# Kernel tuning notes

Hardware: AMD Instinct MI355X
Metric: run time of the kernel (lower is better)

## Reference

```python
import jax, jax.numpy as jnp
import numpy as np

S, B, E = 1024, 64, 1024   # src_seq_len, batch, encoder_hidden_size
H, A = 1024, 1024          # decoder hidden, attention dim
EMB, V = 512, 32000        # embedding_dim, output vocab


def setup_inputs() -> dict:
    key = jax.random.key(0)
    ks = jax.random.split(key, 16)
    sd = lambda n: 1.0 / np.sqrt(n)
    u = lambda k, shape, n: jax.random.uniform(k, shape, jnp.float32, -sd(n), sd(n))
    return {
        "prev_y": jax.random.normal(ks[0], (B, EMB), jnp.float32),
        "prev_h": jax.random.normal(ks[1], (1, B, H), jnp.float32),
        "enc_out": jax.random.normal(ks[2], (S, B, E), jnp.float32),
        # attention params
        "U_w": u(ks[3], (A, E), E), "U_b": u(ks[4], (A,), E),
        "W_w": u(ks[5], (A, H), H), "W_b": u(ks[6], (A,), H),
        "v_w": u(ks[7], (1, A), A), "v_b": u(ks[8], (1,), A),
        # combine + GRU + output params
        "Wc_w": u(ks[9], (H, EMB + E), EMB + E), "Wc_b": u(ks[10], (H,), EMB + E),
        "W_ih": u(ks[11], (3 * H, H), H), "W_hh": u(ks[12], (3 * H, H), H),
        "b_ih": u(ks[13], (3 * H,), H), "b_hh": u(ks[14], (3 * H,), H),
        "Wout_w": u(ks[15], (V, H), H), "Wout_b": jnp.zeros((V,), jnp.float32),
        "mask": 768,
    }


def reference(prev_y, prev_h, enc_out, U_w, U_b, W_w, W_b, v_w, v_b,
              Wc_w, Wc_b, W_ih, W_hh, b_ih, b_hh, Wout_w, Wout_b, mask):
    s, b, e = enc_out.shape
    h = prev_h[0]                                     # [B,H]
    # --- additive (Bahdanau) attention with multiplicative 0/1 prefix mask ---
    uh = jnp.einsum('sbe,ae->sba', enc_out, U_w) + U_b  # [S,B,A]
    wq = h @ W_w.T + W_b                                # [B,A]
    scores = (jnp.tanh(uh + wq) @ v_w[0] + v_b[0]).T    # [B,S]
    m = min(int(mask), s)
    mask_vec = (jnp.arange(s) < m).astype(scores.dtype) # [S]
    scores = scores * mask_vec                          # multiply, NOT -inf (faithful)
    attn = jax.nn.softmax(scores, axis=1)               # [B,S]
    ctx = jnp.einsum('bs,sbe->be', attn, enc_out)       # [B,E]
    # --- combine + single GRU step (PyTorch gate order r,z,n) ---
    x = jnp.concatenate([prev_y, ctx], axis=1) @ Wc_w.T + Wc_b  # [B,H]
    gi = x @ W_ih.T + b_ih                              # [B,3H]
    gh = h @ W_hh.T + b_hh
    Hh = h.shape[1]
    r = jax.nn.sigmoid(gi[:, :Hh] + gh[:, :Hh])
    z = jax.nn.sigmoid(gi[:, Hh:2 * Hh] + gh[:, Hh:2 * Hh])
    n = jnp.tanh(gi[:, 2 * Hh:] + r * gh[:, 2 * Hh:])
    h_new = (1.0 - z) * n + z * h                       # [B,H]
    # --- output projection + log-softmax ---
    logits = h_new @ Wout_w.T + Wout_b                  # [B,V]
    dec_output = jax.nn.log_softmax(logits, axis=1)
    return dec_output, h_new[None], attn
```

## Files before the change

kernel.cpp:

```cpp
#include <hip/hip_runtime.h>

typedef float f32x4 __attribute__((ext_vector_type(4)));
typedef short short8 __attribute__((ext_vector_type(8)));

#define SEQ   1024
#define BB    64
#define VOCAB 32000

__device__ __forceinline__ unsigned short f2bf(float f){
  union { float f; unsigned u; } v; v.f = f;
  unsigned r = v.u + 0x7FFFu + ((v.u >> 16) & 1u);
  return (unsigned short)(r >> 16);
}
__device__ __forceinline__ unsigned pk2(float a, float b){
  return (unsigned)f2bf(a) | ((unsigned)f2bf(b) << 16);
}
__device__ __forceinline__ float tanh_fast(float x){
  float a = fminf(fmaxf(x, -15.f), 15.f);
  float e = __expf(2.f * a);
  return (e - 1.f) / (e + 1.f);
}
__device__ __forceinline__ float sigm(float x){ return 1.f / (1.f + expf(-x)); }

__device__ __forceinline__ void ld4(float4* dst, const float* p){
  const float4* q = (const float4*)p;
  dst[0]=q[0]; dst[1]=q[1]; dst[2]=q[2]; dst[3]=q[3];
}
__device__ __forceinline__ void cvt_store(char* base, int row, int kb0, const float4* f){
  int xs = (row & 7) << 4;
  uint4 u;
  u.x = pk2(f[0].x, f[0].y); u.y = pk2(f[0].z, f[0].w);
  u.z = pk2(f[1].x, f[1].y); u.w = pk2(f[1].z, f[1].w);
  *(uint4*)(base + row*128 + (kb0 ^ xs)) = u;
  u.x = pk2(f[2].x, f[2].y); u.y = pk2(f[2].z, f[2].w);
  u.z = pk2(f[3].x, f[3].y); u.w = pk2(f[3].z, f[3].w);
  *(uint4*)(base + row*128 + ((kb0 + 16) ^ xs)) = u;
}

__global__ __launch_bounds__(256, 2)
void score_gemm(const float* __restrict__ enc, const float* __restrict__ Uw,
                const float* __restrict__ Ub, const float* __restrict__ vw,
                const float* __restrict__ wqm, const int* __restrict__ maskp,
                float* __restrict__ scores)
{
  __shared__ char smem[65536];
  int m = *maskp; m = m < 0 ? 0 : (m > SEQ ? SEQ : m);
  int cx = blockIdx.x & 7, jj = blockIdx.x >> 3;
  int mtile = (jj & ~7) | cx;
  int ntile = jj & 7;
  if (mtile * 2 >= m) return;
  int row0 = mtile * 128;
  int t = threadIdx.x, lane = t & 63;
  int wid = t >> 6, wm = wid >> 1, wn = wid & 1;
  int srow = t >> 2;
  int sk4 = (t & 3) << 4;
  int kb0 = (t & 3) << 5;

  const float* Ag0 = enc + (size_t)(row0 + srow) * 1024 + sk4;
  const float* Ag1 = Ag0 + 64 * 1024;
  const float* Bg0 = Uw  + (size_t)(ntile * 128 + srow) * 1024 + sk4;
  const float* Bg1 = Bg0 + 64 * 1024;

  float4 fa0[4], fa1[4], fb0[4], fb1[4];

  int aAddr[4], bAddr[4], aXor[4], bXor[4];
  #pragma unroll
  for (int i = 0; i < 4; ++i){
    int ra = wm*64 + i*16 + (lane & 15);
    aAddr[i] = ra * 128; aXor[i] = (ra & 7) << 4;
    int rb = wn*64 + i*16 + (lane & 15);
    bAddr[i] = rb * 128; bXor[i] = (rb & 7) << 4;
  }
  int klane = (lane >> 4) << 4;

  f32x4 acc[4][4] = {};

  ld4(fa0, Ag0); ld4(fa1, Ag1); ld4(fb0, Bg0); ld4(fb1, Bg1);
  {
    char* bA = smem; char* bB = smem + 16384;
    cvt_store(bA, srow,      kb0, fa0);
    cvt_store(bA, srow + 64, kb0, fa1);
    cvt_store(bB, srow,      kb0, fb0);
    cvt_store(bB, srow + 64, kb0, fb1);
  }

  #pragma unroll 2
  for (int ks = 0; ks < 16; ++ks){
    int buf = ks & 1;
    if (ks < 15){
      int ko = (ks + 1) * 64;
      ld4(fa0, Ag0 + ko); ld4(fa1, Ag1 + ko);
      ld4(fb0, Bg0 + ko); ld4(fb1, Bg1 + ko);
    }
    __syncthreads();
    {
      char* bA = smem + buf * 32768;
      char* bB = bA + 16384;
      #pragma unroll
      for (int kk = 0; kk < 2; ++kk){
        short8 af[4], bv[4];
        int kb = kk * 64 + klane;
        #pragma unroll
        for (int i = 0; i < 4; ++i){
          af[i] = *(const short8*)(bA + aAddr[i] + (kb ^ aXor[i]));
          bv[i] = *(const short8*)(bB + bAddr[i] + (kb ^ bXor[i]));
        }
        #pragma unroll
        for (int mi = 0; mi < 4; ++mi)
          #pragma unroll
          for (int ni = 0; ni < 4; ++ni)
            acc[mi][ni] = __builtin_amdgcn_mfma_f32_16x16x32_bf16(af[mi], bv[ni], acc[mi][ni], 0, 0, 0);
      }
    }
    if (ks < 15){
      int nb = buf ^ 1;
      char* bA = smem + nb * 32768; char* bB = bA + 16384;
      cvt_store(bA, srow,      kb0, fa0);
      cvt_store(bA, srow + 64, kb0, fa1);
      cvt_store(bB, srow,      kb0, fb0);
      cvt_store(bB, srow + 64, kb0, fb1);
    }
  }

  int s_idx = mtile * 2 + wm;
  if (s_idx < m){
    float ubv[4], vwv[4];
    #pragma unroll
    for (int ni = 0; ni < 4; ++ni){
      int nt = ntile*128 + wn*64 + ni*16 + (lane & 15);
      ubv[ni] = Ub[nt]; vwv[ni] = vw[nt];
    }
    #pragma unroll
    for (int mi = 0; mi < 4; ++mi){
      #pragma unroll
      for (int j = 0; j < 4; ++j){
        int b = mi*16 + ((lane >> 4) << 2) + j;
        const float* wqrow = wqm + b * 1024;
        float asum = 0.f;
        #pragma unroll
        for (int ni = 0; ni < 4; ++ni){
          int nt = ntile*128 + wn*64 + ni*16 + (lane & 15);
          float uh = acc[mi][ni][j] + ubv[ni] + wqrow[nt];
          asum += tanh_fast(uh) * vwv[ni];
        }
        asum += __shfl_xor(asum, 1, 64);
        asum += __shfl_xor(asum, 2, 64);
        asum += __shfl_xor(asum, 4, 64);
        asum += __shfl_xor(asum, 8, 64);
        if ((lane & 15) == 0)
          atomicAdd(scores + b * 1024 + s_idx, asum);
      }
    }
  }
}

__global__ __launch_bounds__(256)
void gemm_m64(const float* __restrict__ A, const float* __restrict__ Bw,
              const float* __restrict__ bias, float* __restrict__ C,
              int N, int K, int stepsPerZ)
{
  __shared__ unsigned short sA[2][64 * 40];
  __shared__ unsigned short sB[2][128 * 40];
  int t = threadIdx.x, lane = t & 63, wid = t >> 6;
  int ntile = blockIdx.x, z = blockIdx.z;
  int arow = t >> 2, ak = (t & 3) * 8;
  int brow = t >> 1, bk = (t & 1) * 16;
  const float* Ap = A + (size_t)arow * K + ak + (size_t)z * stepsPerZ * 32;
  const float* Bp = Bw + (size_t)(ntile * 128 + brow) * K + bk + (size_t)z * stepsPerZ * 32;
  int klane = (lane >> 4) << 4;
  f32x4 acc[4][2] = {};
  float4 a0, a1, b0, b1, b2, b3;

  {
    const float4* pa = (const float4*)Ap;
    a0 = pa[0]; a1 = pa[1];
    const float4* pb = (const float4*)Bp;
    b0 = pb[0]; b1 = pb[1]; b2 = pb[2]; b3 = pb[3];
    uint4 u;
    u.x = pk2(a0.x,a0.y); u.y = pk2(a0.z,a0.w);
    u.z = pk2(a1.x,a1.y); u.w = pk2(a1.z,a1.w);
    *(uint4*)((char*)sA[0] + arow*80 + ak*2) = u;
    u.x = pk2(b0.x,b0.y); u.y = pk2(b0.z,b0.w);
    u.z = pk2(b1.x,b1.y); u.w = pk2(b1.z,b1.w);
    *(uint4*)((char*)sB[0] + brow*80 + bk*2) = u;
    u.x = pk2(b2.x,b2.y); u.y = pk2(b2.z,b2.w);
    u.z = pk2(b3.x,b3.y); u.w = pk2(b3.z,b3.w);
    *(uint4*)((char*)sB[0] + brow*80 + bk*2 + 16) = u;
  }

  for (int ks = 0; ks < stepsPerZ; ++ks){
    int buf = ks & 1;
    if (ks + 1 < stepsPerZ){
      int kg = (ks + 1) * 32;
      const float4* pa = (const float4*)(Ap + kg);
      a0 = pa[0]; a1 = pa[1];
      const float4* pb = (const float4*)(Bp + kg);
      b0 = pb[0]; b1 = pb[1]; b2 = pb[2]; b3 = pb[3];
    }
    __syncthreads();
    {
      short8 af[4], bv[2];
      #pragma unroll
      for (int mi = 0; mi < 4; ++mi)
        af[mi] = *(const short8*)((char*)sA[buf] + (mi*16 + (lane & 15))*80 + klane);
      #pragma unroll
      for (int ni = 0; ni < 2; ++ni)
        bv[ni] = *(const short8*)((char*)sB[buf] + (wid*32 + ni*16 + (lane & 15))*80 + klane);
      #pragma unroll
      for (int mi = 0; mi < 4; ++mi)
        #pragma unroll
        for (int ni = 0; ni < 2; ++ni)
          acc[mi][ni] = __builtin_amdgcn_mfma_f32_16x16x32_bf16(af[mi], bv[ni], acc[mi][ni], 0, 0, 0);
    }
    if (ks + 1 < stepsPerZ){
      int nb = buf ^ 1;
      uint4 u;
      u.x = pk2(a0.x,a0.y); u.y = pk2(a0.z,a0.w);
      u.z = pk2(a1.x,a1.y); u.w = pk2(a1.z,a1.w);
      *(uint4*)((char*)sA[nb] + arow*80 + ak*2) = u;
      u.x = pk2(b0.x,b0.y); u.y = pk2(b0.z,b0.w);
      u.z = pk2(b1.x,b1.y); u.w = pk2(b1.z,b1.w);
      *(uint4*)((char*)sB[nb] + brow*80 + bk*2) = u;
      u.x = pk2(b2.x,b2.y); u.y = pk2(b2.z,b2.w);
      u.z = pk2(b3.x,b3.y); u.w = pk2(b3.z,b3.w);
      *(uint4*)((char*)sB[nb] + brow*80 + bk*2 + 16) = u;
    }
  }

  bool multi = (gridDim.z > 1);
  #pragma unroll
  for (int ni = 0; ni < 2; ++ni){
    int cg = ntile*128 + wid*32 + ni*16 + (lane & 15);
    float bz = 0.f;
    if (bias && (!multi || z == 0)) bz = bias[cg];
    #pragma unroll
    for (int mi = 0; mi < 4; ++mi){
      int r0 = mi*16 + ((lane >> 4) << 2);
      #pragma unroll
      for (int j = 0; j < 4; ++j){
        float val = acc[mi][ni][j] + bz;
        int off = (r0 + j) * N + cg;
        if (multi) atomicAdd(C + off, val);
        else       C[off] = val;
      }
    }
  }
}

__global__ __launch_bounds__(256)
void softmax_attn(const float* __restrict__ scores, const float* __restrict__ vb,
                  const int* __restrict__ maskp, float* __restrict__ attn)
{
  __shared__ float sb[4];
  int b = blockIdx.x, t = threadIdx.x, lane = t & 63, wid = t >> 6;
  int m = *maskp; m = m < 0 ? 0 : (m > SEQ ? SEQ : m);
  float vb0 = vb[0];
  float v[4]; float mx = -1e30f;
  #pragma unroll
  for (int k = 0; k < 4; ++k){
    int s = t + k * 256;
    float x = (s < m) ? scores[b*1024 + s] + vb0 : 0.f;
    v[k] = x; mx = fmaxf(mx, x);
  }
  for (int d = 1; d < 64; d <<= 1) mx = fmaxf(mx, __shfl_xor(mx, d, 64));
  if (lane == 0) sb[wid] = mx;
  __syncthreads();
  mx = fmaxf(fmaxf(sb[0], sb[1]), fmaxf(sb[2], sb[3]));
  float sum = 0.f;
  #pragma unroll
  for (int k = 0; k < 4; ++k){ v[k] = expf(v[k] - mx); sum += v[k]; }
  for (int d = 1; d < 64; d <<= 1) sum += __shfl_xor(sum, d, 64);
  __syncthreads();
  if (lane == 0) sb[wid] = sum;
  __syncthreads();
  sum = sb[0] + sb[1] + sb[2] + sb[3];
  #pragma unroll
  for (int k = 0; k < 4; ++k) attn[b*1024 + t + k*256] = v[k] / sum;
}

__global__ __launch_bounds__(256)
void ctx_atomic(const float* __restrict__ attn, const float* __restrict__ enc,
                float* __restrict__ xcat)
{
  int b = blockIdx.x >> 4, ch = blockIdx.x & 15;
  int t = threadIdx.x;
  __shared__ float a_s[64];
  if (t < 64) a_s[t] = attn[b*1024 + ch*64 + t];
  __syncthreads();
  const float* ep = enc + (size_t)(ch * 64) * 65536 + b * 1024 + t * 4;
  f32x4 acc = {};
  for (int s2 = 0; s2 < 64; ++s2){
    f32x4 v = *(const f32x4*)(ep + (size_t)s2 * 65536);
    acc += a_s[s2] * v;
  }
  float* dst = xcat + (size_t)b * 1536 + 512 + t * 4;
  atomicAdd(dst + 0, acc.x);
  atomicAdd(dst + 1, acc.y);
  atomicAdd(dst + 2, acc.z);
  atomicAdd(dst + 3, acc.w);
}

__global__ __launch_bounds__(128)
void copy_py(const float* __restrict__ py, float* __restrict__ xcat)
{
  int b = blockIdx.x, t = threadIdx.x;
  *(f32x4*)(xcat + (size_t)b*1536 + t*4) = *(const f32x4*)(py + (size_t)b*512 + t*4);
}

__global__ __launch_bounds__(256)
void gru_kernel(const float* __restrict__ gi, const float* __restrict__ gh,
                const float* __restrict__ h, float* __restrict__ hnew)
{
  int idx = blockIdx.x * 256 + threadIdx.x;
  int b = idx >> 10, i = idx & 1023;
  const float* gib = gi + b*3072; const float* ghb = gh + b*3072;
  float r = sigm(gib[i] + ghb[i]);
  float z = sigm(gib[1024 + i] + ghb[1024 + i]);
  float n = tanhf(gib[2048 + i] + r * ghb[2048 + i]);
  hnew[idx] = (1.f - z) * n + z * h[idx];
}

__global__ __launch_bounds__(1024)
void logsoftmax_kernel(float* __restrict__ logits)
{
  __shared__ float sb[16];
  int b = blockIdx.x, t = threadIdx.x, lane = t & 63, wid = t >> 6;
  float* row = logits + (size_t)b * VOCAB;
  float v[32]; float mx = -1e30f;
  #pragma unroll
  for (int k = 0; k < 32; ++k){
    int idx = t + k * 1024;
    if (idx < VOCAB){ v[k] = row[idx]; mx = fmaxf(mx, v[k]); }
    else v[k] = -1e30f;
  }
  for (int d = 1; d < 64; d <<= 1) mx = fmaxf(mx, __shfl_xor(mx, d, 64));
  if (lane == 0) sb[wid] = mx;
  __syncthreads();
  float m2 = -1e30f;
  for (int i = 0; i < 16; ++i) m2 = fmaxf(m2, sb[i]);
  mx = m2;
  float sum = 0.f;
  #pragma unroll
  for (int k = 0; k < 32; ++k){
    int idx = t + k * 1024;
    if (idx < VOCAB) sum += expf(v[k] - mx);
  }
  for (int d = 1; d < 64; d <<= 1) sum += __shfl_xor(sum, d, 64);
  __syncthreads();
  if (lane == 0) sb[wid] = sum;
  __syncthreads();
  float s2 = 0.f;
  for (int i = 0; i < 16; ++i) s2 += sb[i];
  float lse = mx + logf(s2);
  #pragma unroll
  for (int k = 0; k < 32; ++k){
    int idx = t + k * 1024;
    if (idx < VOCAB) row[idx] = v[k] - lse;
  }
}

extern "C" void kernel_launch(void* const* d_in, const int* in_sizes, int n_in,
                              void* d_out, int out_size, void* d_ws, size_t ws_size,
                              hipStream_t stream)
{
  const float* prev_y = (const float*)d_in[0];
  const float* prev_h = (const float*)d_in[1];
  const float* enc    = (const float*)d_in[2];
  const float* U_w    = (const float*)d_in[3];
  const float* U_b    = (const float*)d_in[4];
  const float* W_w    = (const float*)d_in[5];
  const float* W_b    = (const float*)d_in[6];
  const float* v_w    = (const float*)d_in[7];
  const float* v_b    = (const float*)d_in[8];
  const float* Wc_w   = (const float*)d_in[9];
  const float* Wc_b   = (const float*)d_in[10];
  const float* W_ih   = (const float*)d_in[11];
  const float* W_hh   = (const float*)d_in[12];
  const float* b_ih   = (const float*)d_in[13];
  const float* b_hh   = (const float*)d_in[14];
  const float* Wout_w = (const float*)d_in[15];
  const float* Wout_b = (const float*)d_in[16];
  const int*   maskp  = (const int*)d_in[17];

  float* ws     = (float*)d_ws;
  float* scores = ws;
  float* wq     = ws + 65536;
  float* xcat   = ws + 131072;
  float* xvec   = ws + 229376;
  float* gi     = ws + 294912;
  float* gh     = ws + 491520;

  float* out_logp = (float*)d_out;
  float* out_h    = out_logp + 64 * VOCAB;
  float* out_attn = out_h + 65536;

  hipMemsetAsync(d_ws, 0, (size_t)688128 * sizeof(float), stream);

  gemm_m64<<<dim3(8, 1, 8), 256, 0, stream>>>(prev_h, W_w, W_b, wq, 1024, 1024, 4);
  score_gemm<<<4096, 256, 0, stream>>>(enc, U_w, U_b, v_w, wq, maskp, scores);
  softmax_attn<<<64, 256, 0, stream>>>(scores, v_b, maskp, out_attn);
  ctx_atomic<<<1024, 256, 0, stream>>>(out_attn, enc, xcat);
  copy_py<<<64, 128, 0, stream>>>(prev_y, xcat);
  gemm_m64<<<dim3(8, 1, 8), 256, 0, stream>>>(xcat, Wc_w, Wc_b, xvec, 1024, 1536, 6);
  gemm_m64<<<dim3(24, 1, 8), 256, 0, stream>>>(xvec, W_ih, b_ih, gi, 3072, 1024, 4);
  gemm_m64<<<dim3(24, 1, 8), 256, 0, stream>>>(prev_h, W_hh, b_hh, gh, 3072, 1024, 4);
  gru_kernel<<<256, 256, 0, stream>>>(gi, gh, prev_h, out_h);
  gemm_m64<<<dim3(250, 1, 1), 256, 0, stream>>>(out_h, Wout_w, Wout_b, out_logp, VOCAB, 1024, 32);
  logsoftmax_kernel<<<64, 1024, 0, stream>>>(out_logp);
}
```

Measured before the change: 827.0 us.

## Pre-convert enc/U_w to bf16, use direct LDS loads, replace atomics with partial buffers

```diff
diff --git a/kernel.cpp b/kernel.cpp
--- a/kernel.cpp
+++ b/kernel.cpp
@@ -2,9 +2,9 @@
 
 typedef float f32x4 __attribute__((ext_vector_type(4)));
 typedef short short8 __attribute__((ext_vector_type(8)));
+typedef unsigned int u32;
 
 #define SEQ   1024
-#define BB    64
 #define VOCAB 32000
 
 __device__ __forceinline__ unsigned short f2bf(float f){
@@ -14,6 +14,9 @@
 }
 __device__ __forceinline__ unsigned pk2(float a, float b){
   return (unsigned)f2bf(a) | ((unsigned)f2bf(b) << 16);
+}
+__device__ __forceinline__ float bf2f(unsigned short h){
+  union { unsigned u; float f; } v; v.u = ((unsigned)h) << 16; return v.f;
 }
 __device__ __forceinline__ float tanh_fast(float x){
   float a = fminf(fmaxf(x, -15.f), 15.f);
@@ -36,32 +39,48 @@
   u.z = pk2(f[3].x, f[3].y); u.w = pk2(f[3].z, f[3].w);
   *(uint4*)(base + row*128 + ((kb0 + 16) ^ xs)) = u;
 }
-
-__global__ __launch_bounds__(256, 2)
-void score_gemm(const float* __restrict__ enc, const float* __restrict__ Uw,
-                const float* __restrict__ Ub, const float* __restrict__ vw,
-                const float* __restrict__ wqm, const int* __restrict__ maskp,
-                float* __restrict__ scores)
-{
-  __shared__ char smem[65536];
+__device__ __forceinline__ void gload_lds16(const void* g, void* l){
+  __builtin_amdgcn_global_load_lds((const __attribute__((address_space(1))) u32*)g,
+                                   (__attribute__((address_space(3))) u32*)l, 16, 0, 0);
+}
+
+__global__ __launch_bounds__(256)
+void convert_all(const float* __restrict__ uw, const float* __restrict__ enc,
+                 unsigned short* __restrict__ uwb, unsigned short* __restrict__ encb)
+{
+  const int UWC = 131072;
+  const int TOT = UWC + 8388608;
+  int stride = gridDim.x * 256;
+  for (int c = blockIdx.x*256 + threadIdx.x; c < TOT; c += stride){
+    const float* src; unsigned short* dst;
+    if (c < UWC){ src = uw + (size_t)c*8;        dst = uwb + (size_t)c*8; }
+    else        { size_t e = (size_t)(c-UWC)*8;  src = enc + e; dst = encb + e; }
+    float4 f0 = ((const float4*)src)[0], f1 = ((const float4*)src)[1];
+    uint4 u;
+    u.x = pk2(f0.x,f0.y); u.y = pk2(f0.z,f0.w);
+    u.z = pk2(f1.x,f1.y); u.w = pk2(f1.z,f1.w);
+    *(uint4*)dst = u;
+  }
+}
+
+__global__ __launch_bounds__(256)
+void score_gemm_bf16(const unsigned short* __restrict__ encb,
+                     const unsigned short* __restrict__ uwb,
+                     const float* __restrict__ Ub, const float* __restrict__ vw,
+                     const float* __restrict__ wqm, const int* __restrict__ maskp,
+                     float* __restrict__ scores_part)
+{
+  __shared__ char smem[32768];
   int m = *maskp; m = m < 0 ? 0 : (m > SEQ ? SEQ : m);
-  int cx = blockIdx.x & 7, jj = blockIdx.x >> 3;
-  int mtile = (jj & ~7) | cx;
-  int ntile = jj & 7;
+  int bI = blockIdx.x;
+  int mtile = bI & 511, ntile = bI >> 9;
   if (mtile * 2 >= m) return;
-  int row0 = mtile * 128;
-  int t = threadIdx.x, lane = t & 63;
-  int wid = t >> 6, wm = wid >> 1, wn = wid & 1;
-  int srow = t >> 2;
-  int sk4 = (t & 3) << 4;
-  int kb0 = (t & 3) << 5;
-
-  const float* Ag0 = enc + (size_t)(row0 + srow) * 1024 + sk4;
-  const float* Ag1 = Ag0 + 64 * 1024;
-  const float* Bg0 = Uw  + (size_t)(ntile * 128 + srow) * 1024 + sk4;
-  const float* Bg1 = Bg0 + 64 * 1024;
-
-  float4 fa0[4], fa1[4], fb0[4], fb1[4];
+  int t = threadIdx.x, lane = t & 63, wid = t >> 6;
+  int wm = wid >> 1, wn = wid & 1;
+
+  int cswz = (((lane & 7) ^ (lane >> 3)) << 4);
+  const char* pa = (const char*)encb + ((size_t)(mtile*128 + wid*8 + (lane>>3)))*2048 + cswz;
+  const char* pb = (const char*)uwb  + ((size_t)(ntile*128 + wid*8 + (lane>>3)))*2048 + cswz;
 
   int aAddr[4], bAddr[4], aXor[4], bXor[4];
   #pragma unroll
@@ -74,51 +93,30 @@
   int klane = (lane >> 4) << 4;
 
   f32x4 acc[4][4] = {};
-
-  ld4(fa0, Ag0); ld4(fa1, Ag1); ld4(fb0, Bg0); ld4(fb1, Bg1);
-  {
-    char* bA = smem; char* bB = smem + 16384;
-    cvt_store(bA, srow,      kb0, fa0);
-    cvt_store(bA, srow + 64, kb0, fa1);
-    cvt_store(bB, srow,      kb0, fb0);
-    cvt_store(bB, srow + 64, kb0, fb1);
-  }
-
-  #pragma unroll 2
+  char* bA = smem; char* bB = smem + 16384;
+
   for (int ks = 0; ks < 16; ++ks){
-    int buf = ks & 1;
-    if (ks < 15){
-      int ko = (ks + 1) * 64;
-      ld4(fa0, Ag0 + ko); ld4(fa1, Ag1 + ko);
-      ld4(fb0, Bg0 + ko); ld4(fb1, Bg1 + ko);
-    }
     __syncthreads();
-    {
-      char* bA = smem + buf * 32768;
-      char* bB = bA + 16384;
-      #pragma unroll
-      for (int kk = 0; kk < 2; ++kk){
-        short8 af[4], bv[4];
-        int kb = kk * 64 + klane;
+    #pragma unroll
+    for (int i = 0; i < 4; ++i){
+      gload_lds16(pa + (size_t)i*65536 + ks*128, bA + (i*4 + wid)*1024);
+      gload_lds16(pb + (size_t)i*65536 + ks*128, bB + (i*4 + wid)*1024);
+    }
+    __syncthreads();
+    #pragma unroll
+    for (int kk = 0; kk < 2; ++kk){
+      short8 af[4], bv[4];
+      int kb = kk * 64 + klane;
+      #pragma unroll
+      for (int i = 0; i < 4; ++i){
+        af[i] = *(const short8*)(bA + aAddr[i] + (kb ^ aXor[i]));
+        bv[i] = *(const short8*)(bB + bAddr[i] + (kb ^ bXor[i]));
+      }
+      #pragma unroll
+      for (int mi = 0; mi < 4; ++mi)
         #pragma unroll
-        for (int i = 0; i < 4; ++i){
-          af[i] = *(const short8*)(bA + aAddr[i] + (kb ^ aXor[i]));
-          bv[i] = *(const short8*)(bB + bAddr[i] + (kb ^ bXor[i]));
-        }
-        #pragma unroll
-        for (int mi = 0; mi < 4; ++mi)
-          #pragma unroll
-          for (int ni = 0; ni < 4; ++ni)
-            acc[mi][ni] = __builtin_amdgcn_mfma_f32_16x16x32_bf16(af[mi], bv[ni], acc[mi][ni], 0, 0, 0);
-      }
-    }
-    if (ks < 15){
-      int nb = buf ^ 1;
-      char* bA = smem + nb * 32768; char* bB = bA + 16384;
-      cvt_store(bA, srow,      kb0, fa0);
-      cvt_store(bA, srow + 64, kb0, fa1);
-      cvt_store(bB, srow,      kb0, fb0);
-      cvt_store(bB, srow + 64, kb0, fb1);
+        for (int ni = 0; ni < 4; ++ni)
+          acc[mi][ni] = __builtin_amdgcn_mfma_f32_16x16x32_bf16(af[mi], bv[ni], acc[mi][ni], 0, 0, 0);
     }
   }
 
@@ -148,7 +146,120 @@
         asum += __shfl_xor(asum, 4, 64);
         asum += __shfl_xor(asum, 8, 64);
         if ((lane & 15) == 0)
-          atomicAdd(scores + b * 1024 + s_idx, asum);
+          scores_part[(ntile*2 + wn)*65536 + s_idx*64 + b] = asum;
+      }
+    }
+  }
+}
+
+__global__ __launch_bounds__(256, 2)
+void score_gemm_f32(const float* __restrict__ enc, const float* __restrict__ Uw,
+                    const float* __restrict__ Ub, const float* __restrict__ vw,
+                    const float* __restrict__ wqm, const int* __restrict__ maskp,
+                    float* __restrict__ scores_part)
+{
+  __shared__ char smem[65536];
+  int m = *maskp; m = m < 0 ? 0 : (m > SEQ ? SEQ : m);
+  int bI = blockIdx.x;
+  int mtile = bI & 511, ntile = bI >> 9;
+  if (mtile * 2 >= m) return;
+  int row0 = mtile * 128;
+  int t = threadIdx.x, lane = t & 63;
+  int wid = t >> 6, wm = wid >> 1, wn = wid & 1;
+  int srow = t >> 2;
+  int sk4 = (t & 3) << 4;
+  int kb0 = (t & 3) << 5;
+
+  const float* Ag0 = enc + (size_t)(row0 + srow) * 1024 + sk4;
+  const float* Ag1 = Ag0 + 64 * 1024;
+  const float* Bg0 = Uw  + (size_t)(ntile * 128 + srow) * 1024 + sk4;
+  const float* Bg1 = Bg0 + 64 * 1024;
+
+  float4 fa0[4], fa1[4], fb0[4], fb1[4];
+  int aAddr[4], bAddr[4], aXor[4], bXor[4];
+  #pragma unroll
+  for (int i = 0; i < 4; ++i){
+    int ra = wm*64 + i*16 + (lane & 15);
+    aAddr[i] = ra * 128; aXor[i] = (ra & 7) << 4;
+    int rb = wn*64 + i*16 + (lane & 15);
+    bAddr[i] = rb * 128; bXor[i] = (rb & 7) << 4;
+  }
+  int klane = (lane >> 4) << 4;
+  f32x4 acc[4][4] = {};
+
+  ld4(fa0, Ag0); ld4(fa1, Ag1); ld4(fb0, Bg0); ld4(fb1, Bg1);
+  {
+    char* bA = smem; char* bB = smem + 16384;
+    cvt_store(bA, srow,      kb0, fa0);
+    cvt_store(bA, srow + 64, kb0, fa1);
+    cvt_store(bB, srow,      kb0, fb0);
+    cvt_store(bB, srow + 64, kb0, fb1);
+  }
+  #pragma unroll 2
+  for (int ks = 0; ks < 16; ++ks){
+    int buf = ks & 1;
+    if (ks < 15){
+      int ko = (ks + 1) * 64;
+      ld4(fa0, Ag0 + ko); ld4(fa1, Ag1 + ko);
+      ld4(fb0, Bg0 + ko); ld4(fb1, Bg1 + ko);
+    }
+    __syncthreads();
+    {
+      char* bA = smem + buf * 32768;
+      char* bB = bA + 16384;
+      #pragma unroll
+      for (int kk = 0; kk < 2; ++kk){
+        short8 af[4], bv[4];
+        int kb = kk * 64 + klane;
+        #pragma unroll
+        for (int i = 0; i < 4; ++i){
+          af[i] = *(const short8*)(bA + aAddr[i] + (kb ^ aXor[i]));
+          bv[i] = *(const short8*)(bB + bAddr[i] + (kb ^ bXor[i]));
+        }
+        #pragma unroll
+        for (int mi = 0; mi < 4; ++mi)
+          #pragma unroll
+          for (int ni = 0; ni < 4; ++ni)
+            acc[mi][ni] = __builtin_amdgcn_mfma_f32_16x16x32_bf16(af[mi], bv[ni], acc[mi][ni], 0, 0, 0);
+      }
+    }
+    if (ks < 15){
+      int nb = buf ^ 1;
+      char* bA = smem + nb * 32768; char* bB = bA + 16384;
+      cvt_store(bA, srow,      kb0, fa0);
+      cvt_store(bA, srow + 64, kb0, fa1);
+      cvt_store(bB, srow,      kb0, fb0);
+      cvt_store(bB, srow + 64, kb0, fb1);
+    }
+  }
+
+  int s_idx = mtile * 2 + wm;
+  if (s_idx < m){
+    float ubv[4], vwv[4];
+    #pragma unroll
+    for (int ni = 0; ni < 4; ++ni){
+      int nt = ntile*128 + wn*64 + ni*16 + (lane & 15);
+      ubv[ni] = Ub[nt]; vwv[ni] = vw[nt];
+    }
+    #pragma unroll
+    for (int mi = 0; mi < 4; ++mi){
+      #pragma unroll
+      for (int j = 0; j < 4; ++j){
+        int b = mi*16 + ((lane >> 4) << 2) + j;
+        const float* wqrow = wqm + b * 1024;
+        float asum = 0.f;
+        #pragma unroll
+        for (int ni = 0; ni < 4; ++ni){
+          int nt = ntile*128 + wn*64 + ni*16 + (lane & 15);
+          float uh = acc[mi][ni][j] + ubv[ni] + wqrow[nt];
+          asum += tanh_fast(uh) * vwv[ni];
+        }
+        asum += __shfl_xor(asum, 1, 64);
+        asum += __shfl_xor(asum, 2, 64);
+        asum += __shfl_xor(asum, 4, 64);
+        asum += __shfl_xor(asum, 8, 64);
+        if ((lane & 15) == 0)
+          scores_part[(ntile*2 + wn)*65536 + s_idx*64 + b] = asum;
       }
     }
   }
@@ -157,7 +268,7 @@
 __global__ __launch_bounds__(256)
 void gemm_m64(const float* __restrict__ A, const float* __restrict__ Bw,
               const float* __restrict__ bias, float* __restrict__ C,
-              int N, int K, int stepsPerZ)
+              float* __restrict__ Cpart, int N, int K, int stepsPerZ)
 {
   __shared__ unsigned short sA[2][64 * 40];
   __shared__ unsigned short sB[2][128 * 40];
@@ -231,24 +342,35 @@
   #pragma unroll
   for (int ni = 0; ni < 2; ++ni){
     int cg = ntile*128 + wid*32 + ni*16 + (lane & 15);
-    float bz = 0.f;
-    if (bias && (!multi || z == 0)) bz = bias[cg];
+    float bz = (bias && !multi) ? bias[cg] : 0.f;
     #pragma unroll
     for (int mi = 0; mi < 4; ++mi){
       int r0 = mi*16 + ((lane >> 4) << 2);
       #pragma unroll
       for (int j = 0; j < 4; ++j){
         float val = acc[mi][ni][j] + bz;
-        int off = (r0 + j) * N + cg;
-        if (multi) atomicAdd(C + off, val);
-        else       C[off] = val;
+        if (multi) Cpart[((size_t)z*64 + r0 + j)*N + cg] = val;
+        else       C[(size_t)(r0 + j)*N + cg] = val;
       }
     }
   }
 }
 
 __global__ __launch_bounds__(256)
-void softmax_attn(const float* __restrict__ scores, const float* __restrict__ vb,
+void reduce8_bias(const float* __restrict__ part, const float* __restrict__ bias,
+                  float* __restrict__ out, int N)
+{
+  int idx = blockIdx.x*256 + threadIdx.x;
+  int r = idx / (N >> 2), c4 = (idx % (N >> 2)) * 4;
+  f32x4 acc = *(const f32x4*)(bias + c4);
+  #pragma unroll
+  for (int z = 0; z < 8; ++z)
+    acc += *(const f32x4*)(part + ((size_t)z*64 + r)*N + c4);
+  *(f32x4*)(out + (size_t)r*N + c4) = acc;
+}
+
+__global__ __launch_bounds__(256)
+void softmax_attn(const float* __restrict__ sp, const float* __restrict__ vb,
                   const int* __restrict__ maskp, float* __restrict__ attn)
 {
   __shared__ float sb[4];
@@ -259,7 +381,13 @@
   #pragma unroll
   for (int k = 0; k < 4; ++k){
     int s = t + k * 256;
-    float x = (s < m) ? scores[b*1024 + s] + vb0 : 0.f;
+    float x = 0.f;
+    if (s < m){
+      float a = 0.f;
+      #pragma unroll
+      for (int p = 0; p < 16; ++p) a += sp[p*65536 + s*64 + b];
+      x = a + vb0;
+    }
     v[k] = x; mx = fmaxf(mx, x);
   }
   for (int d = 1; d < 64; d <<= 1) mx = fmaxf(mx, __shfl_xor(mx, d, 64));
@@ -279,8 +407,28 @@
 }
 
 __global__ __launch_bounds__(256)
-void ctx_atomic(const float* __restrict__ attn, const float* __restrict__ enc,
-                float* __restrict__ xcat)
+void ctx_bf16(const float* __restrict__ attn, const unsigned short* __restrict__ encb,
+              float* __restrict__ ctx_part)
+{
+  int b = blockIdx.x >> 4, ch = blockIdx.x & 15;
+  int t = threadIdx.x;
+  __shared__ float a_s[64];
+  if (t < 64) a_s[t] = attn[b*1024 + ch*64 + t];
+  __syncthreads();
+  const unsigned short* base = encb + ((size_t)(ch*64)*64 + b)*1024 + t*4;
+  f32x4 acc = {};
+  for (int s2 = 0; s2 < 64; ++s2){
+    ushort4 vv = *(const ushort4*)(base + (size_t)s2*65536);
+    float w = a_s[s2];
+    acc.x += w * bf2f(vv.x); acc.y += w * bf2f(vv.y);
+    acc.z += w * bf2f(vv.z); acc.w += w * bf2f(vv.w);
+  }
+  *(f32x4*)(ctx_part + (size_t)(b*16 + ch)*1024 + t*4) = acc;
+}
+
+__global__ __launch_bounds__(256)
+void ctx_f32(const float* __restrict__ attn, const float* __restrict__ enc,
+             float* __restrict__ ctx_part)
 {
   int b = blockIdx.x >> 4, ch = blockIdx.x & 15;
   int t = threadIdx.x;
@@ -293,31 +441,43 @@
     f32x4 v = *(const f32x4*)(ep + (size_t)s2 * 65536);
     acc += a_s[s2] * v;
   }
-  float* dst = xcat + (size_t)b * 1536 + 512 + t * 4;
-  atomicAdd(dst + 0, acc.x);
-  atomicAdd(dst + 1, acc.y);
-  atomicAdd(dst + 2, acc.z);
-  atomicAdd(dst + 3, acc.w);
-}
-
-__global__ __launch_bounds__(128)
-void copy_py(const float* __restrict__ py, float* __restrict__ xcat)
+  *(f32x4*)(ctx_part + (size_t)(b*16 + ch)*1024 + t*4) = acc;
+}
+
+__global__ __launch_bounds__(256)
+void build_xcat(const float* __restrict__ part, const float* __restrict__ py,
+                float* __restrict__ xcat)
 {
   int b = blockIdx.x, t = threadIdx.x;
-  *(f32x4*)(xcat + (size_t)b*1536 + t*4) = *(const f32x4*)(py + (size_t)b*512 + t*4);
-}
-
-__global__ __launch_bounds__(256)
-void gru_kernel(const float* __restrict__ gi, const float* __restrict__ gh,
-                const float* __restrict__ h, float* __restrict__ hnew)
+  f32x4 acc = {};
+  #pragma unroll
+  for (int c2 = 0; c2 < 16; ++c2)
+    acc += *(const f32x4*)(part + (size_t)(b*16 + c2) * 1024 + t * 4);
+  *(f32x4*)(xcat + b*1536 + 512 + t*4) = acc;
+  if (t < 128)
+    *(f32x4*)(xcat + b*1536 + t*4) = *(const f32x4*)(py + b*512 + t*4);
+}
+
+__global__ __launch_bounds__(256)
+void gru_fused(const float* __restrict__ gip, const float* __restrict__ ghp,
+               const float* __restrict__ b_ih, const float* __restrict__ b_hh,
+               const float* __restrict__ h, float* __restrict__ hnew)
 {
   int idx = blockIdx.x * 256 + threadIdx.x;
   int b = idx >> 10, i = idx & 1023;
-  const float* gib = gi + b*3072; const float* ghb = gh + b*3072;
-  float r = sigm(gib[i] + ghb[i]);
-  float z = sigm(gib[1024 + i] + ghb[1024 + i]);
-  float n = tanhf(gib[2048 + i] + r * ghb[2048 + i]);
-  hnew[idx] = (1.f - z) * n + z * h[idx];
+  float gr = b_ih[i], gz = b_ih[1024+i], gn = b_ih[2048+i];
+  float hr = b_hh[i], hz = b_hh[1024+i], hn = b_hh[2048+i];
+  #pragma unroll
+  for (int z = 0; z < 8; ++z){
+    const float* p = gip + (size_t)z*196608 + b*3072;
+    gr += p[i]; gz += p[1024+i]; gn += p[2048+i];
+    const float* q = ghp + (size_t)z*196608 + b*3072;
+    hr += q[i]; hz += q[1024+i]; hn += q[2048+i];
+  }
+  float r  = sigm(gr + hr);
+  float zz = sigm(gz + hz);
+  float n  = tanhf(gn + r * hn);
+  hnew[idx] = (1.f - zz) * n + zz * h[idx];
 }
 
 __global__ __launch_bounds__(1024)
@@ -382,29 +542,53 @@
   const float* Wout_b = (const float*)d_in[16];
   const int*   maskp  = (const int*)d_in[17];
 
-  float* ws     = (float*)d_ws;
-  float* scores = ws;
-  float* wq     = ws + 65536;
-  float* xcat   = ws + 131072;
-  float* xvec   = ws + 229376;
-  float* gi     = ws + 294912;
-  float* gh     = ws + 491520;
+  char* wsb = (char*)d_ws;
+  const size_t ENC_B = 134217728ULL;
+  const size_t UW_B  = 2097152ULL;
+  const size_t FLOATS_B = 26083328ULL;
+  bool big = ws_size >= ENC_B + UW_B + FLOATS_B;
+
+  unsigned short* encb = (unsigned short*)wsb;
+  unsigned short* uwb  = (unsigned short*)(wsb + ENC_B);
+  float* f = (float*)(wsb + (big ? (ENC_B + UW_B) : 0));
+  float* scores_part = f;
+  float* wq_part     = scores_part + 1048576;
+  float* wq          = wq_part + 524288;
+  float* ctx_part    = wq + 65536;
+  float* xcat        = ctx_part + 1048576;
+  float* xvec_part   = xcat + 98304;
+  float* xvec        = xvec_part + 524288;
+  float* gi_part     = xvec + 65536;
+  float* gh_part     = gi_part + 1572864;
 
   float* out_logp = (float*)d_out;
   float* out_h    = out_logp + 64 * VOCAB;
   float* out_attn = out_h + 65536;
 
-  hipMemsetAsync(d_ws, 0, (size_t)688128 * sizeof(float), stream);
-
-  gemm_m64<<<dim3(8, 1, 8), 256, 0, stream>>>(prev_h, W_w, W_b, wq, 1024, 1024, 4);
-  score_gemm<<<4096, 256, 0, stream>>>(enc, U_w, U_b, v_w, wq, maskp, scores);
-  softmax_attn<<<64, 256, 0, stream>>>(scores, v_b, maskp, out_attn);
-  ctx_atomic<<<1024, 256, 0, stream>>>(out_attn, enc, xcat);
-  copy_py<<<64, 128, 0, stream>>>(prev_y, xcat);
-  gemm_m64<<<dim3(8, 1, 8), 256, 0, stream>>>(xcat, Wc_w, Wc_b, xvec, 1024, 1536, 6);
-  gemm_m64<<<dim3(24, 1, 8), 256, 0, stream>>>(xvec, W_ih, b_ih, gi, 3072, 1024, 4);
-  gemm_m64<<<dim3(24, 1, 8), 256, 0, stream>>>(prev_h, W_hh, b_hh, gh, 3072, 1024, 4);
-  gru_kernel<<<256, 256, 0, stream>>>(gi, gh, prev_h, out_h);
-  gemm_m64<<<dim3(250, 1, 1), 256, 0, stream>>>(out_h, Wout_w, Wout_b, out_logp, VOCAB, 1024, 32);
+  if (big)
+    convert_all<<<2048, 256, 0, stream>>>(U_w, enc, uwb, encb);
+
+  gemm_m64<<<dim3(8,1,8), 256, 0, stream>>>(prev_h, W_w, nullptr, nullptr, wq_part, 1024, 1024, 4);
+  reduce8_bias<<<64, 256, 0, stream>>>(wq_part, W_b, wq, 1024);
+
+  if (big)
+    score_gemm_bf16<<<4096, 256, 0, stream>>>(encb, uwb, U_b, v_w, wq, maskp, scores_part);
+  else
+    score_gemm_f32<<<4096, 256, 0, stream>>>(enc, U_w, U_b, v_w, wq, maskp, scores_part);
+
+  softmax_attn<<<64, 256, 0, stream>>>(scores_part, v_b, maskp, out_attn);
+
+  if (big) ctx_bf16<<<1024, 256, 0, stream>>>(out_attn, encb, ctx_part);
+  else     ctx_f32<<<1024, 256, 0, stream>>>(out_attn, enc, ctx_part);
+  build_xcat<<<64, 256, 0, stream>>>(ctx_part, prev_y, xcat);
+
+  gemm_m64<<<dim3(8,1,8), 256, 0, stream>>>(xcat, Wc_w, nullptr, nullptr, xvec_part, 1024, 1536, 6);
+  reduce8_bias<<<64, 256, 0, stream>>>(xvec_part, Wc_b, xvec, 1024);
+
+  gemm_m64<<<dim3(24,1,8), 256, 0, stream>>>(xvec, W_ih, nullptr, nullptr, gi_part, 3072, 1024, 4);
+  gemm_m64<<<dim3(24,1,8), 256, 0, stream>>>(prev_h, W_hh, nullptr, nullptr, gh_part, 3072, 1024, 4);
+  gru_fused<<<256, 256, 0, stream>>>(gi_part, gh_part, b_ih, b_hh, prev_h, out_h);
+
+  gemm_m64<<<dim3(250,1,1), 256, 0, stream>>>(out_h, Wout_w, Wout_b, out_logp, nullptr, VOCAB, 1024, 32);
   logsoftmax_kernel<<<64, 1024, 0, stream>>>(out_logp);
 }
```

After: 806.3 us. -2.5%, faster.
